# Kernel optimization log

Hardware: AMD Instinct MI355X
Metric: run time of the kernel (lower is better)

Reference implementation:

```python
import jax, jax.numpy as jnp
import numpy as np

B, T, E, H, V = 64, 256, 300, 512, 50000
G = 3 * H  # gates: r, z, n (PyTorch order)


def setup_inputs() -> dict:
    key = jax.random.key(0)
    ks = jax.random.split(key, 14)
    k = 1.0 / np.sqrt(H)
    u = lambda kk, sh: jax.random.uniform(kk, sh, jnp.float32, -k, k)
    x = jax.random.randint(ks[0], (B, T), 0, V)
    emb = jax.random.normal(ks[1], (V, E), jnp.float32) * 0.1
    emb = emb.at[0].set(0.0)  # padding_idx=0
    return {
        "x": x,
        "emb": emb,
        # layer 0: input E, both directions stacked on axis 0
        "w_ih0": u(ks[2], (2, G, E)),
        "w_hh0": u(ks[3], (2, G, H)),
        "b_ih0": u(ks[4], (2, G)),
        "b_hh0": u(ks[5], (2, G)),
        # layer 1: input 2H
        "w_ih1": u(ks[6], (2, G, 2 * H)),
        "w_hh1": u(ks[7], (2, G, 2 * H if False else H)) if False else u(ks[7], (2, G, H)),
        "b_ih1": u(ks[8], (2, G)),
        "b_hh1": u(ks[9], (2, G)),
        # classifier
        "w1": u(ks[10], (128, 2 * H)),
        "b1": u(ks[11], (128,)),
        "w2": u(ks[12], (2, 128)),
        "b2": u(ks[13], (2,)),
    }


def _gru_dir(x, w_ih, w_hh, b_ih, b_hh, reverse):
    # x: [B, T, in]; precompute input projections for all timesteps
    xp = jnp.einsum('bti,gi->btg', x, w_ih) + b_ih  # [B, T, 3H]

    def step(h, xp_t):
        gh = h @ w_hh.T + b_hh  # [B, 3H]
        r = jax.nn.sigmoid(xp_t[:, :H] + gh[:, :H])
        z = jax.nn.sigmoid(xp_t[:, H:2 * H] + gh[:, H:2 * H])
        n = jnp.tanh(xp_t[:, 2 * H:] + r * gh[:, 2 * H:])
        h = (1.0 - z) * n + z * h
        return h, h

    h0 = jnp.zeros((x.shape[0], H), x.dtype)
    _, ys = jax.lax.scan(step, h0, jnp.swapaxes(xp, 0, 1), reverse=reverse)
    return jnp.swapaxes(ys, 0, 1)  # [B, T, H], aligned to input positions


def _bigru_layer(x, w_ih, w_hh, b_ih, b_hh):
    f = _gru_dir(x, w_ih[0], w_hh[0], b_ih[0], b_hh[0], False)
    b = _gru_dir(x, w_ih[1], w_hh[1], b_ih[1], b_hh[1], True)
    return jnp.concatenate([f, b], axis=-1)  # [B, T, 2H]


def reference(x, emb, w_ih0, w_hh0, b_ih0, b_hh0, w_ih1, w_hh1, b_ih1, b_hh1, w1, b1, w2, b2):
    e = emb[x]  # [B, T, E]
    h = _bigru_layer(e, w_ih0, w_hh0, b_ih0, b_hh0)
    h = _bigru_layer(h, w_ih1, w_hh1, b_ih1, b_hh1)  # dropout=eval mode (identity)
    pooled = jnp.max(h, axis=1)  # [B, 2H]
    hid = jax.nn.relu(pooled @ w1.T + b1)
    return hid @ w2.T + b2  # [B, 2]
```

## Files before the change

kernel.cpp:

```cpp
#include <hip/hip_runtime.h>

#define BB 64
#define TLEN 256
#define HH 512
#define GG 1536
#define EPAD 320
#define NN 3072
#define MM 16384

typedef __attribute__((ext_vector_type(8))) __fp16 half8;
typedef __attribute__((ext_vector_type(4))) __fp16 half4;
typedef __attribute__((ext_vector_type(4))) float floatx4;

typedef union { unsigned long long u[2]; half8 v; } hpack;
typedef union { half4 h4; unsigned long long u; } hpack4;

__global__ __launch_bounds__(256) void g2_prep(const int* __restrict__ x,
                                               const float* __restrict__ emb,
                                               __fp16* __restrict__ e,
                                               const float* __restrict__ w_ih0,
                                               __fp16* __restrict__ w0p,
                                               const float* __restrict__ w_ih1,
                                               __fp16* __restrict__ w1c) {
  const int blk = blockIdx.x;
  if (blk < 960) {
    int idx = blk * 256 + threadIdx.x;
    int row = idx / 80;
    int c = idx - row * 80;
    half4 v = {0, 0, 0, 0};
    if (c < 75) {
      float4 f = *(const float4*)&w_ih0[(long)row * 300 + c * 4];
      v[0] = (__fp16)f.x; v[1] = (__fp16)f.y; v[2] = (__fp16)f.z; v[3] = (__fp16)f.w;
    }
    *(half4*)&w0p[row * EPAD + c * 4] = v;
  } else if (blk < 2496) {
    long idx = (long)(blk - 960) * 256 + threadIdx.x;
    float4 a = *(const float4*)&w_ih1[idx * 8];
    float4 b = *(const float4*)&w_ih1[idx * 8 + 4];
    half8 o;
    o[0] = (__fp16)a.x; o[1] = (__fp16)a.y; o[2] = (__fp16)a.z; o[3] = (__fp16)a.w;
    o[4] = (__fp16)b.x; o[5] = (__fp16)b.y; o[6] = (__fp16)b.z; o[7] = (__fp16)b.w;
    *(half8*)&w1c[idx * 8] = o;
  } else {
    int idx = (blk - 2496) * 256 + threadIdx.x;
    int row = idx / 80;
    int c = idx - row * 80;
    int t = row >> 6, b = row & 63;
    half4 v = {0, 0, 0, 0};
    if (c < 75) {
      int xi = x[b * TLEN + t];
      float4 f = *(const float4*)&emb[(long)xi * 300 + c * 4];
      v[0] = (__fp16)f.x; v[1] = (__fp16)f.y; v[2] = (__fp16)f.z; v[3] = (__fp16)f.w;
    }
    *(half4*)&e[row * EPAD + c * 4] = v;
  }
}

__global__ __launch_bounds__(256) void g2_gemm(const __fp16* __restrict__ A,
                                               const __fp16* __restrict__ W,
                                               const float* __restrict__ bias,
                                               __fp16* __restrict__ C,
                                               int M, int N, int Kp) {
  __shared__ __fp16 As[128][72];
  __shared__ __fp16 Ws[128][72];
  const int nTiles = N >> 7;
  const int m0 = (blockIdx.x / nTiles) << 7;
  const int n0 = (blockIdx.x % nTiles) << 7;
  const int tid = threadIdx.x;
  const int lane = tid & 63, wv = tid >> 6;
  const int wm = (wv >> 1) << 6, wn = (wv & 1) << 6;
  const int nsub = lane & 15, quad = lane >> 4;

  floatx4 acc[4][4];
#pragma unroll
  for (int i = 0; i < 4; i++)
#pragma unroll
    for (int j = 0; j < 4; j++) acc[i][j] = (floatx4){0.f, 0.f, 0.f, 0.f};

  const int lr = tid >> 3;
  const int lc = (tid & 7) << 3;
  for (int ko = 0; ko < Kp; ko += 64) {
#pragma unroll
    for (int p = 0; p < 4; p++) {
      int r = lr + p * 32;
      *(half8*)&As[r][lc] = *(const half8*)&A[(long)(m0 + r) * Kp + ko + lc];
      *(half8*)&Ws[r][lc] = *(const half8*)&W[(long)(n0 + r) * Kp + ko + lc];
    }
    __syncthreads();
#pragma unroll
    for (int kk = 0; kk < 64; kk += 32) {
      half8 af[4], bf[4];
      const int kr = kk + (quad << 3);
#pragma unroll
      for (int i = 0; i < 4; i++) af[i] = *(const half8*)&As[wm + i * 16 + nsub][kr];
#pragma unroll
      for (int j = 0; j < 4; j++) bf[j] = *(const half8*)&Ws[wn + j * 16 + nsub][kr];
#pragma unroll
      for (int i = 0; i < 4; i++)
#pragma unroll
        for (int j = 0; j < 4; j++)
          acc[i][j] = __builtin_amdgcn_mfma_f32_16x16x32_f16(af[i], bf[j], acc[i][j], 0, 0, 0);
    }
    __syncthreads();
  }
#pragma unroll
  for (int j = 0; j < 4; j++) {
    int col = n0 + wn + j * 16 + nsub;
    float bv = bias[col];
#pragma unroll
    for (int i = 0; i < 4; i++) {
      int rb = m0 + wm + i * 16 + (quad << 2);
#pragma unroll
      for (int ii = 0; ii < 4; ii++)
        C[(long)(rb + ii) * N + col] = (__fp16)(acc[i][j][ii] + bv);
    }
  }
}

__global__ __launch_bounds__(256, 1) void g2_rnn(const float* __restrict__ whh,
                                                 const float* __restrict__ bhh,
                                                 const __fp16* __restrict__ xp,
                                                 __fp16* __restrict__ hout,
                                                 __fp16* __restrict__ hx) {
  __shared__ __fp16 Wl[96][520];
  __shared__ __fp16 hst[4][16][20];
  const unsigned long long SENT = 0xFFFFFFFFFFFFFFFFULL;
  const int bid = blockIdx.x;
  const int gi = bid & 3;
  const int uo = bid >> 2;
  const int d = gi >> 1, g = gi & 1;
  const int tid = threadIdx.x;
  const int lane = tid & 63, wv = tid >> 6;
  const int U0 = uo << 5;
  const int mb = wv & 1, ut = wv >> 1;
  const int nsub = lane & 15, quad = lane >> 4;
  const int bq = (g << 5) + (mb << 4);
  const int ul = (ut << 4) + nsub;

  const float* wd = whh + (long)d * (GG * HH);
  for (int idx = tid; idx < 96 * 64; idx += 256) {
    int r = idx >> 6;
    int c = (idx & 63) << 3;
    int gate = r >> 5, u2 = r & 31;
    const float* src = &wd[(long)(gate * HH + U0 + u2) * HH + c];
    float4 a = *(const float4*)&src[0];
    float4 b = *(const float4*)&src[4];
    half8 o;
    o[0] = (__fp16)a.x; o[1] = (__fp16)a.y; o[2] = (__fp16)a.z; o[3] = (__fp16)a.w;
    o[4] = (__fp16)b.x; o[5] = (__fp16)b.y; o[6] = (__fp16)b.z; o[7] = (__fp16)b.w;
    *(half8*)&Wl[r][c] = o;
  }
  __syncthreads();

  half8 wr_[16], wz_[16], wn_[16];
#pragma unroll
  for (int kk = 0; kk < 16; kk++) {
    const int kcol = (kk << 5) + (quad << 3);
    wr_[kk] = *(const half8*)&Wl[ul][kcol];
    wz_[kk] = *(const half8*)&Wl[32 + ul][kcol];
    wn_[kk] = *(const half8*)&Wl[64 + ul][kcol];
  }

  const float bhr = bhh[d * GG + U0 + ul];
  const float bhz = bhh[d * GG + HH + U0 + ul];
  const float bhn = bhh[d * GG + 2 * HH + U0 + ul];

  const int cidx = ((quad >> 1) << 6) + (nsub << 2) + ((quad & 1) << 1);
  const int pr = lane & 15, pc4 = (lane >> 4) << 2;
  const int pidx = (uo << 7) + (ut << 6) + (pr << 2) + (pc4 >> 2);

  float hprev[4] = {0.f, 0.f, 0.f, 0.f};

  for (int s = 0; s < TLEN; s++) {
    const int tt = d ? (TLEN - 1 - s) : s;
    float xr[4], xz[4], xn[4];
    {
      const __fp16* xb0 = xp + (long)(tt * BB) * NN + d * GG + U0 + ul;
#pragma unroll
      for (int i = 0; i < 4; i++) {
        const __fp16* xb = xb0 + (long)(bq + (quad << 2) + i) * NN;
        xr[i] = (float)xb[0];
        xz[i] = (float)xb[HH];
        xn[i] = (float)xb[2 * HH];
      }
    }
    floatx4 ar0 = {0.f, 0.f, 0.f, 0.f}, ar1 = ar0, az0 = ar0, az1 = ar0, an0 = ar0, an1 = ar0;
    if (s > 0) {
      const int pt = d ? (tt + 1) : (tt - 1);
      const unsigned long long* hx8 =
          (const unsigned long long*)(hx + ((((long)pt * 2 + d) * 2 + g) * 2 + mb) * 8192);
      hpack u[16];
      int bad;
      do {
#pragma unroll
        for (int kk = 0; kk < 16; kk++) {
          u[kk].u[0] = __hip_atomic_load(&hx8[kk * 128 + cidx], __ATOMIC_RELAXED, __HIP_MEMORY_SCOPE_AGENT);
          u[kk].u[1] = __hip_atomic_load(&hx8[kk * 128 + cidx + 1], __ATOMIC_RELAXED, __HIP_MEMORY_SCOPE_AGENT);
        }
        bad = 0;
#pragma unroll
        for (int kk = 0; kk < 16; kk++)
          bad |= (u[kk].u[0] == SENT) | (u[kk].u[1] == SENT);
      } while (__any(bad));
#pragma unroll
      for (int kk = 0; kk < 16; kk += 2) {
        ar0 = __builtin_amdgcn_mfma_f32_16x16x32_f16(u[kk].v, wr_[kk], ar0, 0, 0, 0);
        az0 = __builtin_amdgcn_mfma_f32_16x16x32_f16(u[kk].v, wz_[kk], az0, 0, 0, 0);
        an0 = __builtin_amdgcn_mfma_f32_16x16x32_f16(u[kk].v, wn_[kk], an0, 0, 0, 0);
        ar1 = __builtin_amdgcn_mfma_f32_16x16x32_f16(u[kk + 1].v, wr_[kk + 1], ar1, 0, 0, 0);
        az1 = __builtin_amdgcn_mfma_f32_16x16x32_f16(u[kk + 1].v, wz_[kk + 1], az1, 0, 0, 0);
        an1 = __builtin_amdgcn_mfma_f32_16x16x32_f16(u[kk + 1].v, wn_[kk + 1], an1, 0, 0, 0);
      }
    }
#pragma unroll
    for (int i = 0; i < 4; i++) {
      float grv = ar0[i] + ar1[i] + xr[i] + bhr;
      float gzv = az0[i] + az1[i] + xz[i] + bhz;
      float gnv = an0[i] + an1[i] + bhn;
      float rg = 1.f / (1.f + __expf(-grv));
      float zg = 1.f / (1.f + __expf(-gzv));
      float ex = __expf(2.f * (xn[i] + rg * gnv));
      float ng = 1.f - 2.f / (ex + 1.f);
      float hv = (1.f - zg) * ng + zg * hprev[i];
      hprev[i] = hv;
      hst[wv][(quad << 2) + i][nsub] = (__fp16)hv;
    }
    asm volatile("" ::: "memory");
    {
      hpack4 pk;
      pk.h4 = *(const half4*)&hst[wv][pr][pc4];
      unsigned long long* hxw =
          (unsigned long long*)(hx + ((((long)tt * 2 + d) * 2 + g) * 2 + mb) * 8192);
      __hip_atomic_store(&hxw[pidx], pk.u, __ATOMIC_RELAXED, __HIP_MEMORY_SCOPE_AGENT);
      *(half4*)&hout[(long)(tt * BB + (g << 5) + (mb << 4) + pr) * 1024 +
                     d * HH + U0 + (ut << 4) + pc4] = pk.h4;
    }
  }
}

__global__ __launch_bounds__(256) void g2_pool(const __fp16* __restrict__ h1,
                                               float* __restrict__ pooled) {
  int b = blockIdx.x;
  int j0 = threadIdx.x * 4;
  float m[4] = {-3e38f, -3e38f, -3e38f, -3e38f};
  const __fp16* p = h1 + b * 1024 + j0;
  for (int t = 0; t < TLEN; t++) {
    half4 v = *(const half4*)(p + (long)t * BB * 1024);
#pragma unroll
    for (int q = 0; q < 4; q++) m[q] = fmaxf(m[q], (float)v[q]);
  }
  float* o = pooled + b * 1024 + j0;
#pragma unroll
  for (int q = 0; q < 4; q++) o[q] = m[q];
}

__global__ __launch_bounds__(128) void g2_head(const float* __restrict__ pooled,
                                               const float* __restrict__ w1,
                                               const float* __restrict__ b1,
                                               const float* __restrict__ w2,
                                               const float* __restrict__ b2,
                                               float* __restrict__ out) {
  __shared__ float pl[1024];
  __shared__ float hid[128];
  int b = blockIdx.x, j = threadIdx.x;
  for (int k = j; k < 1024; k += 128) pl[k] = pooled[b * 1024 + k];
  __syncthreads();
  float acc = b1[j];
  const float* wr = w1 + (long)j * 1024;
  for (int k = 0; k < 1024; k += 4) {
    float4 w = *(const float4*)&wr[k];
    acc += pl[k] * w.x + pl[k + 1] * w.y + pl[k + 2] * w.z + pl[k + 3] * w.w;
  }
  hid[j] = fmaxf(acc, 0.f);
  __syncthreads();
  if (j < 2) {
    float a = b2[j];
    for (int k = 0; k < 128; k++) a += hid[k] * w2[j * 128 + k];
    out[b * 2 + j] = a;
  }
}

extern "C" void kernel_launch(void* const* d_in, const int* in_sizes, int n_in,
                              void* d_out, int out_size, void* d_ws, size_t ws_size,
                              hipStream_t stream) {
  (void)in_sizes; (void)n_in; (void)out_size; (void)ws_size;
  const int* x = (const int*)d_in[0];
  const float* emb = (const float*)d_in[1];
  const float* w_ih0 = (const float*)d_in[2];
  const float* w_hh0 = (const float*)d_in[3];
  const float* b_ih0 = (const float*)d_in[4];
  const float* b_hh0 = (const float*)d_in[5];
  const float* w_ih1 = (const float*)d_in[6];
  const float* w_hh1 = (const float*)d_in[7];
  const float* b_ih1 = (const float*)d_in[8];
  const float* b_hh1 = (const float*)d_in[9];
  const float* w1 = (const float*)d_in[10];
  const float* b1 = (const float*)d_in[11];
  const float* w2 = (const float*)d_in[12];
  const float* b2 = (const float*)d_in[13];

  char* ws = (char*)d_ws;
  __fp16* xp = (__fp16*)(ws + 0);
  __fp16* h0 = (__fp16*)(ws + 100663296);
  __fp16* h1 = (__fp16*)(ws + 134217728);
  __fp16* e_pad = (__fp16*)(ws + 167772160);
  __fp16* w0p = (__fp16*)(ws + 178257920);
  __fp16* w1c = (__fp16*)(ws + 180224000);
  float* pooled = (float*)(ws + 186515456);

  (void)hipMemsetAsync(h1, 0xFF, 33554432, stream);
  g2_prep<<<7616, 256, 0, stream>>>(x, emb, e_pad, w_ih0, w0p, w_ih1, w1c);
  g2_gemm<<<3072, 256, 0, stream>>>(e_pad, w0p, b_ih0, xp, MM, NN, EPAD);
  g2_rnn<<<64, 256, 0, stream>>>(w_hh0, b_hh0, xp, h0, h1);
  g2_gemm<<<3072, 256, 0, stream>>>(h0, w1c, b_ih1, xp, MM, NN, 1024);
  (void)hipMemsetAsync(h0, 0xFF, 33554432, stream);
  g2_rnn<<<64, 256, 0, stream>>>(w_hh1, b_hh1, xp, h1, h0);
  g2_pool<<<64, 256, 0, stream>>>(h1, pooled);
  g2_head<<<64, 128, 0, stream>>>(pooled, w1, b1, w2, b2, (float*)d_out);
}
```

Before: 2.046 ms.

## Fuse input-projection GEMM with recurrent kernel via sentinel-polled xp streaming

Merges each layer's input-projection GEMM and GRU recurrence into one launch. The first 64 blocks run the recurrence while the remaining blocks compute GEMM tiles, ordered from both time ends so the forward and backward directions get their rows early. The recurrence polls xp for a sentinel value (xp is memset to 0xFF beforehand) so it can start before the GEMM finishes. It also keeps the r-gate weights in registers and z/n in LDS instead of all in registers, drops the layer-1 hout write, and fuses pool and head to read directly from the hx exchange buffer. The cost is extra 100MB memsets, atomic 8-byte stores, and the risk of deadlock if the persistent blocks are not co-resident with the GEMM blocks.

Measured after the change: 2.298 ms. 12.3% more time.

```diff
diff --git a/kernel.cpp b/kernel.cpp
--- a/kernel.cpp
+++ b/kernel.cpp
@@ -14,6 +14,7 @@
 
 typedef union { unsigned long long u[2]; half8 v; } hpack;
 typedef union { half4 h4; unsigned long long u; } hpack4;
+typedef union { unsigned short s; __fp16 h; } hu16;
 
 __global__ __launch_bounds__(256) void g2_prep(const int* __restrict__ x,
                                                const float* __restrict__ emb,
@@ -56,110 +57,119 @@
   }
 }
 
-__global__ __launch_bounds__(256) void g2_gemm(const __fp16* __restrict__ A,
-                                               const __fp16* __restrict__ W,
-                                               const float* __restrict__ bias,
-                                               __fp16* __restrict__ C,
-                                               int M, int N, int Kp) {
-  __shared__ __fp16 As[128][72];
-  __shared__ __fp16 Ws[128][72];
-  const int nTiles = N >> 7;
-  const int m0 = (blockIdx.x / nTiles) << 7;
-  const int n0 = (blockIdx.x % nTiles) << 7;
-  const int tid = threadIdx.x;
-  const int lane = tid & 63, wv = tid >> 6;
-  const int wm = (wv >> 1) << 6, wn = (wv & 1) << 6;
-  const int nsub = lane & 15, quad = lane >> 4;
-
-  floatx4 acc[4][4];
-#pragma unroll
-  for (int i = 0; i < 4; i++)
-#pragma unroll
-    for (int j = 0; j < 4; j++) acc[i][j] = (floatx4){0.f, 0.f, 0.f, 0.f};
-
-  const int lr = tid >> 3;
-  const int lc = (tid & 7) << 3;
-  for (int ko = 0; ko < Kp; ko += 64) {
-#pragma unroll
-    for (int p = 0; p < 4; p++) {
-      int r = lr + p * 32;
-      *(half8*)&As[r][lc] = *(const half8*)&A[(long)(m0 + r) * Kp + ko + lc];
-      *(half8*)&Ws[r][lc] = *(const half8*)&W[(long)(n0 + r) * Kp + ko + lc];
-    }
-    __syncthreads();
-#pragma unroll
-    for (int kk = 0; kk < 64; kk += 32) {
-      half8 af[4], bf[4];
-      const int kr = kk + (quad << 3);
-#pragma unroll
-      for (int i = 0; i < 4; i++) af[i] = *(const half8*)&As[wm + i * 16 + nsub][kr];
-#pragma unroll
-      for (int j = 0; j < 4; j++) bf[j] = *(const half8*)&Ws[wn + j * 16 + nsub][kr];
-#pragma unroll
-      for (int i = 0; i < 4; i++)
-#pragma unroll
-        for (int j = 0; j < 4; j++)
-          acc[i][j] = __builtin_amdgcn_mfma_f32_16x16x32_f16(af[i], bf[j], acc[i][j], 0, 0, 0);
-    }
-    __syncthreads();
-  }
-#pragma unroll
-  for (int j = 0; j < 4; j++) {
-    int col = n0 + wn + j * 16 + nsub;
-    float bv = bias[col];
-#pragma unroll
-    for (int i = 0; i < 4; i++) {
-      int rb = m0 + wm + i * 16 + (quad << 2);
-#pragma unroll
-      for (int ii = 0; ii < 4; ii++)
-        C[(long)(rb + ii) * N + col] = (__fp16)(acc[i][j][ii] + bv);
-    }
-  }
-}
-
-__global__ __launch_bounds__(256, 1) void g2_rnn(const float* __restrict__ whh,
-                                                 const float* __restrict__ bhh,
-                                                 const __fp16* __restrict__ xp,
-                                                 __fp16* __restrict__ hout,
-                                                 __fp16* __restrict__ hx) {
-  __shared__ __fp16 Wl[96][520];
+__global__ __launch_bounds__(256, 1) void g2_fused(
+    const float* __restrict__ whh,
+    const float* __restrict__ bhh,
+    __fp16* xp,
+    __fp16* __restrict__ hout,
+    __fp16* __restrict__ hx,
+    const __fp16* __restrict__ ga,
+    const __fp16* __restrict__ gw,
+    const float* __restrict__ gbias,
+    int Kp) {
+  __shared__ __align__(16) char smem[65536];
   __shared__ __fp16 hst[4][16][20];
   const unsigned long long SENT = 0xFFFFFFFFFFFFFFFFULL;
   const int bid = blockIdx.x;
+  const int tid = threadIdx.x;
+  const int lane = tid & 63, wv = tid >> 6;
+  const int nsub = lane & 15, quad = lane >> 4;
+
+  if (bid >= 64) {
+    const int gb = bid - 64;
+    const int kb = gb / 24, nb = gb - kb * 24;
+    const int mt = (kb & 1) ? (127 - (kb >> 1)) : (kb >> 1);
+    const int m0 = mt << 7, n0 = nb << 7;
+    __fp16 (*As)[72] = (__fp16(*)[72])smem;
+    __fp16 (*Ws)[72] = (__fp16(*)[72])(smem + 18432);
+    const int wm = (wv >> 1) << 6, wn = (wv & 1) << 6;
+    floatx4 acc[4][4];
+#pragma unroll
+    for (int i = 0; i < 4; i++)
+#pragma unroll
+      for (int j = 0; j < 4; j++) acc[i][j] = (floatx4){0.f, 0.f, 0.f, 0.f};
+    const int lr = tid >> 3;
+    const int lc = (tid & 7) << 3;
+    for (int ko = 0; ko < Kp; ko += 64) {
+#pragma unroll
+      for (int p = 0; p < 4; p++) {
+        int r = lr + p * 32;
+        *(half8*)&As[r][lc] = *(const half8*)&ga[(long)(m0 + r) * Kp + ko + lc];
+        *(half8*)&Ws[r][lc] = *(const half8*)&gw[(long)(n0 + r) * Kp + ko + lc];
+      }
+      __syncthreads();
+#pragma unroll
+      for (int kk = 0; kk < 64; kk += 32) {
+        half8 af[4], bf[4];
+        const int kr = kk + (quad << 3);
+#pragma unroll
+        for (int i = 0; i < 4; i++) af[i] = *(const half8*)&As[wm + i * 16 + nsub][kr];
+#pragma unroll
+        for (int j = 0; j < 4; j++) bf[j] = *(const half8*)&Ws[wn + j * 16 + nsub][kr];
+#pragma unroll
+        for (int i = 0; i < 4; i++)
+#pragma unroll
+          for (int j = 0; j < 4; j++)
+            acc[i][j] = __builtin_amdgcn_mfma_f32_16x16x32_f16(bf[j], af[i], acc[i][j], 0, 0, 0);
+      }
+      __syncthreads();
+    }
+#pragma unroll
+    for (int i = 0; i < 4; i++) {
+      const long row = m0 + wm + i * 16 + nsub;
+#pragma unroll
+      for (int j = 0; j < 4; j++) {
+        const int col = n0 + wn + j * 16 + (quad << 2);
+        const float* bvp = &gbias[col];
+        hpack4 pk;
+#pragma unroll
+        for (int q = 0; q < 4; q++) pk.h4[q] = (__fp16)(acc[i][j][q] + bvp[q]);
+        __hip_atomic_store((unsigned long long*)(xp + row * (long)NN + col), pk.u,
+                           __ATOMIC_RELAXED, __HIP_MEMORY_SCOPE_AGENT);
+      }
+    }
+    return;
+  }
+
   const int gi = bid & 3;
   const int uo = bid >> 2;
   const int d = gi >> 1, g = gi & 1;
-  const int tid = threadIdx.x;
-  const int lane = tid & 63, wv = tid >> 6;
   const int U0 = uo << 5;
   const int mb = wv & 1, ut = wv >> 1;
-  const int nsub = lane & 15, quad = lane >> 4;
   const int bq = (g << 5) + (mb << 4);
   const int ul = (ut << 4) + nsub;
 
-  const float* wd = whh + (long)d * (GG * HH);
-  for (int idx = tid; idx < 96 * 64; idx += 256) {
-    int r = idx >> 6;
-    int c = (idx & 63) << 3;
-    int gate = r >> 5, u2 = r & 31;
-    const float* src = &wd[(long)(gate * HH + U0 + u2) * HH + c];
+  half8 wr_[16];
+  {
+    const float* wrbase = whh + ((long)d * GG + U0 + ul) * HH;
+#pragma unroll
+    for (int kk = 0; kk < 16; kk++) {
+      const float* src = wrbase + (kk << 5) + (quad << 3);
+      float4 a = *(const float4*)&src[0];
+      float4 b = *(const float4*)&src[4];
+      half8 o;
+      o[0] = (__fp16)a.x; o[1] = (__fp16)a.y; o[2] = (__fp16)a.z; o[3] = (__fp16)a.w;
+      o[4] = (__fp16)b.x; o[5] = (__fp16)b.y; o[6] = (__fp16)b.z; o[7] = (__fp16)b.w;
+      wr_[kk] = o;
+    }
+  }
+  half8 (*Wf)[16][64] = (half8(*)[16][64])smem;
+  for (int e = tid; e < 4096; e += 256) {
+    int lane_e = e & 63;
+    int kk = (e >> 6) & 15;
+    int utx = (e >> 10) & 1;
+    int gate = (e >> 11) & 1;
+    int unit = U0 + (utx << 4) + (lane_e & 15);
+    int col = (kk << 5) + ((lane_e >> 4) << 3);
+    const float* src = whh + ((long)d * GG + (gate + 1) * HH + unit) * HH + col;
     float4 a = *(const float4*)&src[0];
     float4 b = *(const float4*)&src[4];
     half8 o;
     o[0] = (__fp16)a.x; o[1] = (__fp16)a.y; o[2] = (__fp16)a.z; o[3] = (__fp16)a.w;
     o[4] = (__fp16)b.x; o[5] = (__fp16)b.y; o[6] = (__fp16)b.z; o[7] = (__fp16)b.w;
-    *(half8*)&Wl[r][c] = o;
+    Wf[gate * 2 + utx][kk][lane_e] = o;
   }
   __syncthreads();
-
-  half8 wr_[16], wz_[16], wn_[16];
-#pragma unroll
-  for (int kk = 0; kk < 16; kk++) {
-    const int kcol = (kk << 5) + (quad << 3);
-    wr_[kk] = *(const half8*)&Wl[ul][kcol];
-    wz_[kk] = *(const half8*)&Wl[32 + ul][kcol];
-    wn_[kk] = *(const half8*)&Wl[64 + ul][kcol];
-  }
 
   const float bhr = bhh[d * GG + U0 + ul];
   const float bhz = bhh[d * GG + HH + U0 + ul];
@@ -168,48 +178,67 @@
   const int cidx = ((quad >> 1) << 6) + (nsub << 2) + ((quad & 1) << 1);
   const int pr = lane & 15, pc4 = (lane >> 4) << 2;
   const int pidx = (uo << 7) + (ut << 6) + (pr << 2) + (pc4 >> 2);
+  const int sh = (nsub & 3) << 4;
 
   float hprev[4] = {0.f, 0.f, 0.f, 0.f};
 
   for (int s = 0; s < TLEN; s++) {
     const int tt = d ? (TLEN - 1 - s) : s;
-    float xr[4], xz[4], xn[4];
-    {
-      const __fp16* xb0 = xp + (long)(tt * BB) * NN + d * GG + U0 + ul;
-#pragma unroll
-      for (int i = 0; i < 4; i++) {
-        const __fp16* xb = xb0 + (long)(bq + (quad << 2) + i) * NN;
-        xr[i] = (float)xb[0];
-        xz[i] = (float)xb[HH];
-        xn[i] = (float)xb[2 * HH];
-      }
-    }
-    floatx4 ar0 = {0.f, 0.f, 0.f, 0.f}, ar1 = ar0, az0 = ar0, az1 = ar0, an0 = ar0, an1 = ar0;
+    const __fp16* xb0 = xp + (long)(tt * BB + bq + (quad << 2)) * NN +
+                        d * GG + U0 + (ut << 4) + (nsub & 12);
+    const unsigned long long* hx8 = 0;
     if (s > 0) {
       const int pt = d ? (tt + 1) : (tt - 1);
-      const unsigned long long* hx8 =
-          (const unsigned long long*)(hx + ((((long)pt * 2 + d) * 2 + g) * 2 + mb) * 8192);
-      hpack u[16];
-      int bad;
-      do {
+      hx8 = (const unsigned long long*)(hx + ((((long)pt * 2 + d) * 2 + g) * 2 + mb) * 8192);
+    }
+    hpack u[16];
+    hpack4 xw[12];
+    int bad;
+    do {
+      if (s > 0) {
 #pragma unroll
         for (int kk = 0; kk < 16; kk++) {
           u[kk].u[0] = __hip_atomic_load(&hx8[kk * 128 + cidx], __ATOMIC_RELAXED, __HIP_MEMORY_SCOPE_AGENT);
           u[kk].u[1] = __hip_atomic_load(&hx8[kk * 128 + cidx + 1], __ATOMIC_RELAXED, __HIP_MEMORY_SCOPE_AGENT);
         }
-        bad = 0;
+      }
+#pragma unroll
+      for (int i = 0; i < 4; i++) {
+        const unsigned long long* q = (const unsigned long long*)(xb0 + (long)i * NN);
+        xw[i * 3 + 0].u = __hip_atomic_load(&q[0], __ATOMIC_RELAXED, __HIP_MEMORY_SCOPE_AGENT);
+        xw[i * 3 + 1].u = __hip_atomic_load(&q[HH / 4], __ATOMIC_RELAXED, __HIP_MEMORY_SCOPE_AGENT);
+        xw[i * 3 + 2].u = __hip_atomic_load(&q[2 * HH / 4], __ATOMIC_RELAXED, __HIP_MEMORY_SCOPE_AGENT);
+      }
+      bad = 0;
+      if (s > 0) {
 #pragma unroll
         for (int kk = 0; kk < 16; kk++)
           bad |= (u[kk].u[0] == SENT) | (u[kk].u[1] == SENT);
-      } while (__any(bad));
+      }
+#pragma unroll
+      for (int w = 0; w < 12; w++) bad |= (xw[w].u == SENT);
+    } while (__any(bad));
+    float xr[4], xz[4], xn[4];
+#pragma unroll
+    for (int i = 0; i < 4; i++) {
+      hu16 t0, t1, t2;
+      t0.s = (unsigned short)(xw[i * 3 + 0].u >> sh);
+      t1.s = (unsigned short)(xw[i * 3 + 1].u >> sh);
+      t2.s = (unsigned short)(xw[i * 3 + 2].u >> sh);
+      xr[i] = (float)t0.h; xz[i] = (float)t1.h; xn[i] = (float)t2.h;
+    }
+    floatx4 ar0 = {0.f, 0.f, 0.f, 0.f}, ar1 = ar0, az0 = ar0, az1 = ar0, an0 = ar0, an1 = ar0;
+    if (s > 0) {
 #pragma unroll
       for (int kk = 0; kk < 16; kk += 2) {
+        half8 wzA = Wf[ut][kk][lane],     wnA = Wf[2 + ut][kk][lane];
+        half8 wzB = Wf[ut][kk + 1][lane], wnB = Wf[2 + ut][kk + 1][lane];
         ar0 = __builtin_amdgcn_mfma_f32_16x16x32_f16(u[kk].v, wr_[kk], ar0, 0, 0, 0);
-        az0 = __builtin_amdgcn_mfma_f32_16x16x32_f16(u[kk].v, wz_[kk], az0, 0, 0, 0);
-        an0 = __builtin_amdgcn_mfma_f32_16x16x32_f16(u[kk].v, wn_[kk], an0, 0, 0, 0);
+        az0 = __builtin_amdgcn_mfma_f32_16x16x32_f16(u[kk].v, wzA, az0, 0, 0, 0);
+        an0 = __builtin_amdgcn_mfma_f32_16x16x32_f16(u[kk].v, wnA, an0, 0, 0, 0);
         ar1 = __builtin_amdgcn_mfma_f32_16x16x32_f16(u[kk + 1].v, wr_[kk + 1], ar1, 0, 0, 0);
-        az1 = __builtin_amdgcn_mfma_f32_16x16x32_f16(u[kk + 1].v, wz_[kk + 1], az1, 0, 0, 0);
-        an1 = __builtin_amdgcn_mfma_f32_16x16x32_f16(u[kk + 1].v, wn_[kk + 1], an1, 0, 0, 0);
+        az1 = __builtin_amdgcn_mfma_f32_16x16x32_f16(u[kk + 1].v, wzB, az1, 0, 0, 0);
+        an1 = __builtin_amdgcn_mfma_f32_16x16x32_f16(u[kk + 1].v, wnB, an1, 0, 0, 0);
       }
     }
 #pragma unroll
@@ -232,51 +261,51 @@
       unsigned long long* hxw =
           (unsigned long long*)(hx + ((((long)tt * 2 + d) * 2 + g) * 2 + mb) * 8192);
       __hip_atomic_store(&hxw[pidx], pk.u, __ATOMIC_RELAXED, __HIP_MEMORY_SCOPE_AGENT);
-      *(half4*)&hout[(long)(tt * BB + (g << 5) + (mb << 4) + pr) * 1024 +
-                     d * HH + U0 + (ut << 4) + pc4] = pk.h4;
+      if (hout)
+        *(half4*)&hout[(long)(tt * BB + (g << 5) + (mb << 4) + pr) * 1024 +
+                       d * HH + U0 + (ut << 4) + pc4] = pk.h4;
     }
   }
 }
 
-__global__ __launch_bounds__(256) void g2_pool(const __fp16* __restrict__ h1,
-                                               float* __restrict__ pooled) {
-  int b = blockIdx.x;
-  int j0 = threadIdx.x * 4;
-  float m[4] = {-3e38f, -3e38f, -3e38f, -3e38f};
-  const __fp16* p = h1 + b * 1024 + j0;
-  for (int t = 0; t < TLEN; t++) {
-    half4 v = *(const half4*)(p + (long)t * BB * 1024);
-#pragma unroll
-    for (int q = 0; q < 4; q++) m[q] = fmaxf(m[q], (float)v[q]);
-  }
-  float* o = pooled + b * 1024 + j0;
-#pragma unroll
-  for (int q = 0; q < 4; q++) o[q] = m[q];
-}
-
-__global__ __launch_bounds__(128) void g2_head(const float* __restrict__ pooled,
-                                               const float* __restrict__ w1,
-                                               const float* __restrict__ b1,
-                                               const float* __restrict__ w2,
-                                               const float* __restrict__ b2,
-                                               float* __restrict__ out) {
+__global__ __launch_bounds__(256) void g2_poolhead(const __fp16* __restrict__ hx1,
+                                                   const float* __restrict__ w1,
+                                                   const float* __restrict__ b1,
+                                                   const float* __restrict__ w2,
+                                                   const float* __restrict__ b2,
+                                                   float* __restrict__ out) {
   __shared__ float pl[1024];
   __shared__ float hid[128];
-  int b = blockIdx.x, j = threadIdx.x;
-  for (int k = j; k < 1024; k += 128) pl[k] = pooled[b * 1024 + k];
+  const int b = blockIdx.x, tid = threadIdx.x;
+  const int dd = tid >> 7;
+  const int j0 = (tid & 127) << 2;
+  const int gg = b >> 5, mbb = (b >> 4) & 1, prr = b & 15;
+  const long ebase = ((long)(dd * 4 + gg * 2 + mbb)) * 8192 +
+                     ((j0 >> 5) << 9) + (((j0 >> 4) & 1) << 8) + (prr << 4) + (j0 & 15);
+  const __fp16* p = hx1 + ebase;
+  float m[4] = {-3e38f, -3e38f, -3e38f, -3e38f};
+  for (int t = 0; t < TLEN; t++) {
+    half4 v = *(const half4*)(p + (long)t * 8 * 8192);
+#pragma unroll
+    for (int q = 0; q < 4; q++) m[q] = fmaxf(m[q], (float)v[q]);
+  }
+#pragma unroll
+  for (int q = 0; q < 4; q++) pl[dd * 512 + j0 + q] = m[q];
   __syncthreads();
-  float acc = b1[j];
-  const float* wr = w1 + (long)j * 1024;
-  for (int k = 0; k < 1024; k += 4) {
-    float4 w = *(const float4*)&wr[k];
-    acc += pl[k] * w.x + pl[k + 1] * w.y + pl[k + 2] * w.z + pl[k + 3] * w.w;
-  }
-  hid[j] = fmaxf(acc, 0.f);
+  if (tid < 128) {
+    float acc = b1[tid];
+    const float* wr = w1 + (long)tid * 1024;
+    for (int k = 0; k < 1024; k += 4) {
+      float4 w = *(const float4*)&wr[k];
+      acc += pl[k] * w.x + pl[k + 1] * w.y + pl[k + 2] * w.z + pl[k + 3] * w.w;
+    }
+    hid[tid] = fmaxf(acc, 0.f);
+  }
   __syncthreads();
-  if (j < 2) {
-    float a = b2[j];
-    for (int k = 0; k < 128; k++) a += hid[k] * w2[j * 128 + k];
-    out[b * 2 + j] = a;
+  if (tid < 2) {
+    float a = b2[tid];
+    for (int k = 0; k < 128; k++) a += hid[k] * w2[tid * 128 + k];
+    out[b * 2 + tid] = a;
   }
 }
 
@@ -306,15 +335,13 @@
   __fp16* e_pad = (__fp16*)(ws + 167772160);
   __fp16* w0p = (__fp16*)(ws + 178257920);
   __fp16* w1c = (__fp16*)(ws + 180224000);
-  float* pooled = (float*)(ws + 186515456);
 
   (void)hipMemsetAsync(h1, 0xFF, 33554432, stream);
+  (void)hipMemsetAsync(xp, 0xFF, 100663296, stream);
   g2_prep<<<7616, 256, 0, stream>>>(x, emb, e_pad, w_ih0, w0p, w_ih1, w1c);
-  g2_gemm<<<3072, 256, 0, stream>>>(e_pad, w0p, b_ih0, xp, MM, NN, EPAD);
-  g2_rnn<<<64, 256, 0, stream>>>(w_hh0, b_hh0, xp, h0, h1);
-  g2_gemm<<<3072, 256, 0, stream>>>(h0, w1c, b_ih1, xp, MM, NN, 1024);
-  (void)hipMemsetAsync(h0, 0xFF, 33554432, stream);
-  g2_rnn<<<64, 256, 0, stream>>>(w_hh1, b_hh1, xp, h1, h0);
-  g2_pool<<<64, 256, 0, stream>>>(h1, pooled);
-  g2_head<<<64, 128, 0, stream>>>(pooled, w1, b1, w2, b2, (float*)d_out);
+  g2_fused<<<3136, 256, 0, stream>>>(w_hh0, b_hh0, xp, h0, h1, e_pad, w0p, b_ih0, EPAD);
+  (void)hipMemsetAsync(h1, 0xFF, 33554432, stream);
+  (void)hipMemsetAsync(xp, 0xFF, 100663296, stream);
+  g2_fused<<<3136, 256, 0, stream>>>(w_hh1, b_hh1, xp, (__fp16*)0, h1, h0, w1c, b_ih1, 1024);
+  g2_poolhead<<<64, 256, 0, stream>>>(h1, w1, b1, w2, b2, (float*)d_out);
 }
```
